# Kernel tuning notes

Measured on AMD Instinct MI355X. Metric: run time of the kernel, lower is better.

Reference implementation:

```python
import jax, jax.numpy as jnp
import numpy as np

EPS = 1e-5

def _ln(x, g=None, b=None):
    m = jnp.mean(x, axis=-1, keepdims=True)
    v = jnp.var(x, axis=-1, keepdims=True)
    y = (x - m) / jnp.sqrt(v + EPS)
    if g is not None:
        y = y * g + b
    return y

def setup_inputs() -> dict:
    key = jax.random.key(0)
    B, N, C = 2, 2048, 1024   # batch, tokens, query_dim
    H, D = 16, 64             # heads, dim_head -> inner = 1024
    inner = H * D
    ks = jax.random.split(key, 8)
    s = C ** -0.5
    inp = {
        'x':   jax.random.normal(ks[0], (B, N, C), jnp.float32),
        'w_q': jax.random.normal(ks[1], (C, inner), jnp.float32) * s,
        'b_q': jnp.zeros((inner,), jnp.float32),
        'w_k': jax.random.normal(ks[2], (C, inner), jnp.float32) * s,
        'b_k': jnp.zeros((inner,), jnp.float32),
        'w_v': jax.random.normal(ks[3], (C, inner), jnp.float32) * s,
        'b_v': jnp.zeros((inner,), jnp.float32),
        'g_q': jnp.ones((inner,), jnp.float32),
        'be_q': jnp.zeros((inner,), jnp.float32),
        'g_k': jnp.ones((inner,), jnp.float32),
        'be_k': jnp.zeros((inner,), jnp.float32),
        # to_out is zero-initialized in the torch code; use small random weights
        # so forward/backward are non-trivial for correctness testing.
        'w_o': jax.random.normal(ks[4], (inner, C), jnp.float32) * s,
        'b_o': jnp.zeros((C,), jnp.float32),
    }
    return inp

def reference(x, w_q, b_q, w_k, b_k, w_v, b_v, g_q, be_q, g_k, be_k, w_o, b_o):
    B, N, C = x.shape
    inner = w_q.shape[1]
    H = 16
    D = inner // H
    xn = _ln(x)                                  # pre-norm, no affine
    ctx = xn                                     # self-attention (context=None)
    silu = jax.nn.silu
    q = silu(xn) @ w_q + b_q                     # [B,N,inner]
    k = silu(ctx) @ w_k + b_k
    v = silu(ctx) @ w_v + b_v
    q = _ln(q, g_q, be_q)
    k = _ln(k, g_k, be_k)
    q = q * (inner ** -0.5)                      # NB: scale by inner_dim, pre-split
    q = q.reshape(B, N, H, D)
    k = k.reshape(B, N, H, D)
    v = v.reshape(B, N, H, D)
    w = jnp.einsum('bihd,bjhd->bhij', q, k)      # [B,H,N,N]
    w = jax.nn.softmax(w, axis=-1)
    o = jnp.einsum('bhij,bjhd->bihd', w, v).reshape(B, N, inner)
    return silu(o) @ w_o + b_o
```

## Files before the change

### kernel.cpp

```cpp
#include <hip/hip_runtime.h>
#include <hip/hip_bf16.h>
#include <math.h>

#define LN_EPS 1e-5f

typedef __attribute__((ext_vector_type(8))) short bf16x8;
typedef __attribute__((ext_vector_type(8))) short short8;
typedef __attribute__((ext_vector_type(4))) float f32x4;
typedef unsigned short ushort_t;

__device__ __forceinline__ float silu_f(float x) {
    return x / (1.0f + __expf(-x));
}

__device__ __forceinline__ ushort_t f2bf(float f) {
    __hip_bfloat16 h = __float2bfloat16(f);
    return *reinterpret_cast<ushort_t*>(&h);
}

__device__ __forceinline__ float bf2f(ushort_t u) {
    __hip_bfloat16 h = *reinterpret_cast<__hip_bfloat16*>(&u);
    return __bfloat162float(h);
}

__device__ __forceinline__ unsigned pk2(float a, float b) {
#if defined(__has_builtin)
#if __has_builtin(__builtin_amdgcn_cvt_pk_bf16_f32)
    return __builtin_bit_cast(unsigned, __builtin_amdgcn_cvt_pk_bf16_f32(a, b));
#else
    return (((unsigned)f2bf(b)) << 16) | (unsigned)f2bf(a);
#endif
#else
    return (((unsigned)f2bf(b)) << 16) | (unsigned)f2bf(a);
#endif
}

__device__ __forceinline__ void gld16(const void* g, void* lds) {
    __builtin_amdgcn_global_load_lds(
        (const __attribute__((address_space(1))) unsigned int*)g,
        (__attribute__((address_space(3))) unsigned int*)lds, 16, 0, 0);
}

__device__ __forceinline__ float2 block_reduce2(float2 p, float2* sbuf) {
    #pragma unroll
    for (int off = 32; off > 0; off >>= 1) {
        p.x += __shfl_down(p.x, off, 64);
        p.y += __shfl_down(p.y, off, 64);
    }
    int lane = threadIdx.x & 63;
    int wid  = threadIdx.x >> 6;
    if (lane == 0) sbuf[wid] = p;
    __syncthreads();
    if (threadIdx.x == 0) {
        float2 r = sbuf[0];
        for (int i = 1; i < 4; ++i) { r.x += sbuf[i].x; r.y += sbuf[i].y; }
        sbuf[0] = r;
    }
    __syncthreads();
    return sbuf[0];
}

__global__ __launch_bounds__(256) void ln_silu_kernel(
    const float* __restrict__ x, ushort_t* __restrict__ out)
{
    __shared__ float2 sbuf[4];
    const int C = 1024;
    int row = blockIdx.x;
    const float4* xr = (const float4*)(x + (size_t)row * C);
    float4 v = xr[threadIdx.x];
    float2 p;
    p.x = v.x + v.y + v.z + v.w;
    p.y = v.x*v.x + v.y*v.y + v.z*v.z + v.w*v.w;
    float2 s = block_reduce2(p, sbuf);
    float mean = s.x / (float)C;
    float var  = s.y / (float)C - mean * mean;
    float rstd = rsqrtf(var + LN_EPS);
    ushort4 y;
    y.x = f2bf(silu_f((v.x - mean) * rstd));
    y.y = f2bf(silu_f((v.y - mean) * rstd));
    y.z = f2bf(silu_f((v.z - mean) * rstd));
    y.w = f2bf(silu_f((v.w - mean) * rstd));
    ((ushort4*)(out + (size_t)row * C))[threadIdx.x] = y;
}

__global__ __launch_bounds__(256) void ln_affine_bf16(
    ushort_t* __restrict__ qk0, ushort_t* __restrict__ qk1,
    const float* __restrict__ g0, const float* __restrict__ be0,
    const float* __restrict__ g1, const float* __restrict__ be1,
    float scale0, float scale1)
{
    __shared__ float2 sbuf[4];
    const int C = 1024;
    int which = blockIdx.y;
    ushort_t* q = which ? qk1 : qk0;
    const float* g  = which ? g1  : g0;
    const float* be = which ? be1 : be0;
    float scale = which ? scale1 : scale0;
    int row = blockIdx.x;
    ushort4 u = ((ushort4*)(q + (size_t)row * C))[threadIdx.x];
    float v0 = bf2f(u.x), v1 = bf2f(u.y), v2 = bf2f(u.z), v3 = bf2f(u.w);
    float2 p;
    p.x = v0 + v1 + v2 + v3;
    p.y = v0*v0 + v1*v1 + v2*v2 + v3*v3;
    float2 s = block_reduce2(p, sbuf);
    float mean = s.x / (float)C;
    float var  = s.y / (float)C - mean * mean;
    float rstd = rsqrtf(var + LN_EPS);
    float4 gv = ((const float4*)g)[threadIdx.x];
    float4 bv = ((const float4*)be)[threadIdx.x];
    ushort4 y;
    y.x = f2bf(((v0 - mean) * rstd * gv.x + bv.x) * scale);
    y.y = f2bf(((v1 - mean) * rstd * gv.y + bv.y) * scale);
    y.z = f2bf(((v2 - mean) * rstd * gv.z + bv.z) * scale);
    y.w = f2bf(((v3 - mean) * rstd * gv.w + bv.w) * scale);
    ((ushort4*)(q + (size_t)row * C))[threadIdx.x] = y;
}

struct W4 { const float* p[4]; };

__global__ __launch_bounds__(256) void transpose_w(W4 w, ushort_t* __restrict__ outbase)
{
    __shared__ float Ls[64][65];
    int z = blockIdx.z;
    const float* in = w.p[z];
    ushort_t* out = outbase + (size_t)z * 1024 * 1024;
    int r0 = blockIdx.y * 64, c0 = blockIdx.x * 64;
    int t = threadIdx.x, r = t >> 2, j = (t & 3) * 16;
    #pragma unroll
    for (int i = 0; i < 4; ++i) {
        float4 v = *(const float4*)(in + (size_t)(r0 + r) * 1024 + c0 + j + i * 4);
        Ls[r][j + i*4 + 0] = v.x;
        Ls[r][j + i*4 + 1] = v.y;
        Ls[r][j + i*4 + 2] = v.z;
        Ls[r][j + i*4 + 3] = v.w;
    }
    __syncthreads();
    __align__(16) ushort_t tmp[16];
    #pragma unroll
    for (int i = 0; i < 16; ++i) tmp[i] = f2bf(Ls[j + i][r]);
    ushort_t* op = out + (size_t)(c0 + r) * 1024 + r0 + j;
    *(short8*)(op)     = *(short8*)(tmp);
    *(short8*)(op + 8) = *(short8*)(tmp + 8);
}

template<int BM, bool OUT_BF16>
__global__ __launch_bounds__(256) void gemm_mfma(
    const ushort_t* __restrict__ A, const ushort_t* __restrict__ Bt0,
    const float* __restrict__ b0, const float* __restrict__ b1,
    const float* __restrict__ b2, void* __restrict__ out0,
    ushort_t* __restrict__ vt_out,
    int M, int N, int K)
{
    constexpr int BK = 64;
    constexpr int MI = BM / 32;
    __shared__ ushort_t Smem[(BM + 128) * BK];
    ushort_t* As = Smem;
    ushort_t* Bs = Smem + BM * BK;

    int z = blockIdx.z;
    const ushort_t* Bt = Bt0 + (size_t)z * N * K;
    const float* bias = (z == 0) ? b0 : (z == 1) ? b1 : b2;

    int t = threadIdx.x;
    int lane = t & 63, wv = t >> 6;
    int wr = wv >> 1, wc = wv & 1;
    int quad = lane >> 4, ln16 = lane & 15;

    int row0 = blockIdx.y * BM;
    int col0 = blockIdx.x * 128;

    const f32x4 zero4 = {0.f, 0.f, 0.f, 0.f};
    f32x4 acc[MI][4];
    #pragma unroll
    for (int i = 0; i < MI; ++i)
        #pragma unroll
        for (int j = 0; j < 4; ++j) acc[i][j] = zero4;

    for (int kt = 0; kt < K; kt += BK) {
        #pragma unroll
        for (int c = 0; c < BM / 32; ++c) {
            int idx = c * 256 + t;
            int r = idx >> 3, ch = idx & 7;
            int g = ch ^ (r & 7);
            gld16(A + (size_t)(row0 + r) * K + kt + g * 8,
                  As + (size_t)(c * 256 + wv * 64) * 8);
        }
        #pragma unroll
        for (int c = 0; c < 4; ++c) {
            int idx = c * 256 + t;
            int r = idx >> 3, ch = idx & 7;
            int g = ch ^ (r & 7);
            gld16(Bt + (size_t)(col0 + r) * K + kt + g * 8,
                  Bs + (size_t)(c * 256 + wv * 64) * 8);
        }
        __syncthreads();
        #pragma unroll
        for (int s = 0; s < 2; ++s) {
            bf16x8 af[MI], bf[4];
            int g = s * 4 + quad;
            #pragma unroll
            for (int i = 0; i < MI; ++i) {
                int m = wr * (BM / 2) + i * 16 + ln16;
                af[i] = *(const bf16x8*)(As + (size_t)(m * 8 + (g ^ (m & 7))) * 8);
            }
            #pragma unroll
            for (int j = 0; j < 4; ++j) {
                int n = wc * 64 + j * 16 + ln16;
                bf[j] = *(const bf16x8*)(Bs + (size_t)(n * 8 + (g ^ (n & 7))) * 8);
            }
            #pragma unroll
            for (int i = 0; i < MI; ++i)
                #pragma unroll
                for (int j = 0; j < 4; ++j)
                    acc[i][j] = __builtin_amdgcn_mfma_f32_16x16x32_bf16(
                        af[i], bf[j], acc[i][j], 0, 0, 0);
        }
        __syncthreads();
    }

    if (OUT_BF16 && z == 2 && BM == 128) {
        ushort_t* tb = Smem + wv * 4096;
        int tok0 = row0 + wr * 64;
        int chn0 = col0 + wc * 64;
        #pragma unroll
        for (int j = 0; j < 4; ++j) {
            int chl = j * 16 + ln16;
            float bv = bias[chn0 + chl];
            #pragma unroll
            for (int i = 0; i < MI; ++i) {
                uint2 uu;
                uu.x = pk2(acc[i][j][0] + bv, acc[i][j][1] + bv);
                uu.y = pk2(acc[i][j][2] + bv, acc[i][j][3] + bv);
                int hc = i * 4 + quad;
                int phys = hc ^ ((chl & 7) << 1);
                *(uint2*)(tb + chl * 64 + phys * 4) = uu;
            }
        }
        int bb2 = tok0 >> 11;
        int tokb = tok0 & 2047;
        #pragma unroll
        for (int p = 0; p < 8; ++p) {
            int chl = p * 8 + (lane >> 3);
            int tc  = lane & 7;
            int ptc = tc ^ (chl & 7);
            uint4 vvv = *(const uint4*)(tb + chl * 64 + ptc * 8);
            *(uint4*)(vt_out + ((size_t)bb2 * 1024 + chn0 + chl) * 2048 + tokb + tc * 8) = vvv;
        }
    } else {
        #pragma unroll
        for (int j = 0; j < 4; ++j) {
            int col = col0 + wc * 64 + j * 16 + ln16;
            float bv = bias[col];
            #pragma unroll
            for (int i = 0; i < MI; ++i) {
                int rowb = row0 + wr * (BM / 2) + i * 16 + quad * 4;
                #pragma unroll
                for (int r = 0; r < 4; ++r) {
                    float val = acc[i][j][r] + bv;
                    if (OUT_BF16) {
                        ushort_t* out = (ushort_t*)out0 + (size_t)z * M * N;
                        out[(size_t)(rowb + r) * N + col] = f2bf(val);
                    } else {
                        float* out = (float*)out0;
                        out[(size_t)(rowb + r) * N + col] = val;
                    }
                }
            }
        }
    }
}

__global__ __launch_bounds__(256, 4) void flash_mfma(
    const ushort_t* __restrict__ qb, const ushort_t* __restrict__ kb,
    const ushort_t* __restrict__ vT, ushort_t* __restrict__ ob)
{
    const int N = 2048, HD = 1024, D = 64, H = 16;
    const int KT = 64;
    const int NT = N / KT;
    __shared__ ushort_t Ks[2][64 * 64];
    __shared__ ushort_t Vs[2][64 * 64];

    int t = threadIdx.x, lane = t & 63, wv = t >> 6;
    int quad = lane >> 4, ln16 = lane & 15;
    int qt = blockIdx.x, h = blockIdx.y, b = blockIdx.z;

    size_t qk_base = (size_t)b * N * HD + (size_t)h * D;
    size_t vt_base = (size_t)(b * H + h) * D * N;

    bf16x8 qf[2];
    {
        const ushort_t* qp = qb + qk_base + (size_t)(qt * 64 + wv * 16 + ln16) * HD;
        qf[0] = *(const bf16x8*)(qp + quad * 8);
        qf[1] = *(const bf16x8*)(qp + 32 + quad * 8);
    }

    const f32x4 zero4 = {0.f, 0.f, 0.f, 0.f};
    f32x4 oacc[4];
    #pragma unroll
    for (int j = 0; j < 4; ++j) oacc[j] = zero4;
    float lcur = 0.f;

    auto stage_tile = [&](ushort_t* KsB, ushort_t* VsB, int kt) {
        #pragma unroll
        for (int c = 0; c < 2; ++c) {
            int idx = c * 256 + t;
            int r = idx >> 3, ch = idx & 7, g = ch ^ (r & 7);
            int pr = (r & ~31) | (((r >> 2) & 3) << 3) | (((r >> 4) & 1) << 2) | (r & 3);
            gld16(kb + qk_base + (size_t)(kt + pr) * HD + g * 8,
                  KsB + (size_t)(c * 256 + wv * 64) * 8);
        }
        #pragma unroll
        for (int c = 0; c < 2; ++c) {
            int idx = c * 256 + t;
            int r = idx >> 3, ch = idx & 7, g = ch ^ (r & 7);
            gld16(vT + vt_base + (size_t)r * N + kt + g * 8,
                  VsB + (size_t)(c * 256 + wv * 64) * 8);
        }
    };

    auto compute_tile = [&](const ushort_t* KsB, const ushort_t* VsB) {
        f32x4 st[4];
        #pragma unroll
        for (int j = 0; j < 4; ++j) st[j] = zero4;
        __builtin_amdgcn_s_setprio(1);
        #pragma unroll
        for (int s = 0; s < 2; ++s) {
            int g = s * 4 + quad;
            #pragma unroll
            for (int j = 0; j < 4; ++j) {
                int n = j * 16 + ln16;
                bf16x8 kf = *(const bf16x8*)(KsB + ((size_t)n * 8 + (g ^ (n & 7))) * 8);
                st[j] = __builtin_amdgcn_mfma_f32_16x16x32_bf16(kf, qf[s], st[j], 0, 0, 0);
            }
        }
        __builtin_amdgcn_s_setprio(0);

        #pragma unroll
        for (int j = 0; j < 4; ++j) {
            st[j][0] = exp2f(st[j][0]);
            st[j][1] = exp2f(st[j][1]);
            st[j][2] = exp2f(st[j][2]);
            st[j][3] = exp2f(st[j][3]);
            lcur += (st[j][0] + st[j][1]) + (st[j][2] + st[j][3]);
        }

        #pragma unroll
        for (int w = 0; w < 2; ++w) {
            uint4 up;
            up.x = pk2(st[2*w][0],   st[2*w][1]);
            up.y = pk2(st[2*w][2],   st[2*w][3]);
            up.z = pk2(st[2*w+1][0], st[2*w+1][1]);
            up.w = pk2(st[2*w+1][2], st[2*w+1][3]);
            bf16x8 pf = __builtin_bit_cast(bf16x8, up);
            int lc = w * 4 + quad;
            int phys = lc ^ (ln16 & 7);
            __builtin_amdgcn_s_setprio(1);
            #pragma unroll
            for (int mt = 0; mt < 4; ++mt) {
                int dd = mt * 16 + ln16;
                bf16x8 vf = *(const bf16x8*)(VsB + (size_t)dd * 64 + phys * 8);
                oacc[mt] = __builtin_amdgcn_mfma_f32_16x16x32_bf16(vf, pf, oacc[mt], 0, 0, 0);
            }
            __builtin_amdgcn_s_setprio(0);
        }
        __builtin_amdgcn_sched_barrier(0);
    };

    stage_tile(Ks[0], Vs[0], 0);
    #pragma unroll 1
    for (int it = 0; it < NT; it += 2) {
        stage_tile(Ks[1], Vs[1], (it + 1) * KT);
        asm volatile("s_waitcnt vmcnt(4)" ::: "memory");
        __builtin_amdgcn_s_barrier();
        __builtin_amdgcn_sched_barrier(0);
        compute_tile(Ks[0], Vs[0]);
        __builtin_amdgcn_s_barrier();

        if (it + 2 < NT) {
            stage_tile(Ks[0], Vs[0], (it + 2) * KT);
            asm volatile("s_waitcnt vmcnt(4)" ::: "memory");
        } else {
            asm volatile("s_waitcnt vmcnt(0)" ::: "memory");
        }
        __builtin_amdgcn_s_barrier();
        __builtin_amdgcn_sched_barrier(0);
        compute_tile(Ks[1], Vs[1]);
        __builtin_amdgcn_s_barrier();
    }

    lcur += __shfl_xor(lcur, 16, 64);
    lcur += __shfl_xor(lcur, 32, 64);

    float inv = 1.0f / lcur;
    size_t rowoff = qk_base + (size_t)(qt * 64 + wv * 16 + ln16) * HD;
    #pragma unroll
    for (int mt = 0; mt < 4; ++mt) {
        float o0 = silu_f(oacc[mt][0] * inv);
        float o1 = silu_f(oacc[mt][1] * inv);
        float o2 = silu_f(oacc[mt][2] * inv);
        float o3 = silu_f(oacc[mt][3] * inv);
        uint2 uu;
        uu.x = pk2(o0, o1);
        uu.y = pk2(o2, o3);
        *(uint2*)(ob + rowoff + mt * 16 + quad * 4) = uu;
    }
}

extern "C" void kernel_launch(void* const* d_in, const int* in_sizes, int n_in,
                              void* d_out, int out_size, void* d_ws, size_t ws_size,
                              hipStream_t stream) {
    const float* x    = (const float*)d_in[0];
    const float* w_q  = (const float*)d_in[1];
    const float* b_q  = (const float*)d_in[2];
    const float* w_k  = (const float*)d_in[3];
    const float* b_k  = (const float*)d_in[4];
    const float* w_v  = (const float*)d_in[5];
    const float* b_v  = (const float*)d_in[6];
    const float* g_q  = (const float*)d_in[7];
    const float* be_q = (const float*)d_in[8];
    const float* g_k  = (const float*)d_in[9];
    const float* be_k = (const float*)d_in[10];
    const float* w_o  = (const float*)d_in[11];
    const float* b_o  = (const float*)d_in[12];
    float* out = (float*)d_out;

    const int B = 2, N = 2048, C = 1024, H = 16, INNER = 1024;
    const int M = B * N;
    const size_t MC = (size_t)M * C;

    ushort_t* ws  = (ushort_t*)d_ws;
    ushort_t* sx  = ws;
    ushort_t* qkv = ws + MC;
    ushort_t* vTp = ws + 4 * MC;
    ushort_t* wT  = ws + 5 * MC;

    ushort_t* qbuf = qkv;
    ushort_t* kbuf = qkv + MC;
    ushort_t* obuf = sx;

    W4 w4; w4.p[0] = w_q; w4.p[1] = w_k; w4.p[2] = w_v; w4.p[3] = w_o;
    transpose_w<<<dim3(16, 16, 4), 256, 0, stream>>>(w4, wT);

    ln_silu_kernel<<<M, 256, 0, stream>>>(x, sx);

    gemm_mfma<128, true><<<dim3(INNER / 128, M / 128, 3), 256, 0, stream>>>(
        sx, wT, b_q, b_k, b_v, qkv, vTp, M, INNER, C);

    ln_affine_bf16<<<dim3(M, 2), 256, 0, stream>>>(
        qbuf, kbuf, g_q, be_q, g_k, be_k, 0.03125f * 1.44269504f, 1.0f);

    flash_mfma<<<dim3(N / 64, H, B), 256, 0, stream>>>(qbuf, kbuf, vTp, obuf);

    gemm_mfma<64, false><<<dim3(C / 128, M / 64, 1), 256, 0, stream>>>(
        obuf, wT + (size_t)3 * 1024 * 1024, b_o, b_o, b_o, out, nullptr, M, C, INNER);
}
```

Baseline: 240.8 us.

## Process two query sub-tiles per wave and compute row sums via MFMA

Each wave now handles 32 query rows instead of 16, so every K and V fragment read from LDS is reused for two MFMAs, and each block covers 128 queries. This halves the grid and the K/V staging traffic per query. The softmax denominator is now accumulated with an MFMA against a ones vector on the bf16-rounded probabilities, replacing the VALU adds and cross-lane shuffles. Register pressure roughly doubles, so launch bounds drop to 2 blocks per SM. The grid also falls to 512 blocks, which may reduce occupancy and latency hiding.

```diff
diff --git a/kernel.cpp b/kernel.cpp
--- a/kernel.cpp
+++ b/kernel.cpp
@@ -270,7 +270,7 @@
     }
 }
 
-__global__ __launch_bounds__(256, 4) void flash_mfma(
+__global__ __launch_bounds__(256, 2) void flash_mfma(
     const ushort_t* __restrict__ qb, const ushort_t* __restrict__ kb,
     const ushort_t* __restrict__ vT, ushort_t* __restrict__ ob)
 {
@@ -287,18 +287,28 @@
     size_t qk_base = (size_t)b * N * HD + (size_t)h * D;
     size_t vt_base = (size_t)(b * H + h) * D * N;
 
-    bf16x8 qf[2];
-    {
-        const ushort_t* qp = qb + qk_base + (size_t)(qt * 64 + wv * 16 + ln16) * HD;
-        qf[0] = *(const bf16x8*)(qp + quad * 8);
-        qf[1] = *(const bf16x8*)(qp + 32 + quad * 8);
-    }
+    bf16x8 qf[2][2];
+    #pragma unroll
+    for (int u = 0; u < 2; ++u) {
+        const ushort_t* qp = qb + qk_base +
+            (size_t)(qt * 128 + wv * 32 + u * 16 + ln16) * HD;
+        qf[u][0] = *(const bf16x8*)(qp + quad * 8);
+        qf[u][1] = *(const bf16x8*)(qp + 32 + quad * 8);
+    }
+
+    bf16x8 ones;
+    #pragma unroll
+    for (int i = 0; i < 8; ++i) ones[i] = (short)0x3F80;
 
     const f32x4 zero4 = {0.f, 0.f, 0.f, 0.f};
-    f32x4 oacc[4];
-    #pragma unroll
-    for (int j = 0; j < 4; ++j) oacc[j] = zero4;
-    float lcur = 0.f;
+    f32x4 oacc[2][4];
+    f32x4 lacc[2];
+    #pragma unroll
+    for (int u = 0; u < 2; ++u) {
+        lacc[u] = zero4;
+        #pragma unroll
+        for (int j = 0; j < 4; ++j) oacc[u][j] = zero4;
+    }
 
     auto stage_tile = [&](ushort_t* KsB, ushort_t* VsB, int kt) {
         #pragma unroll
@@ -319,9 +329,11 @@
     };
 
     auto compute_tile = [&](const ushort_t* KsB, const ushort_t* VsB) {
-        f32x4 st[4];
-        #pragma unroll
-        for (int j = 0; j < 4; ++j) st[j] = zero4;
+        f32x4 st[2][4];
+        #pragma unroll
+        for (int u = 0; u < 2; ++u)
+            #pragma unroll
+            for (int j = 0; j < 4; ++j) st[u][j] = zero4;
         __builtin_amdgcn_s_setprio(1);
         #pragma unroll
         for (int s = 0; s < 2; ++s) {
@@ -330,36 +342,45 @@
             for (int j = 0; j < 4; ++j) {
                 int n = j * 16 + ln16;
                 bf16x8 kf = *(const bf16x8*)(KsB + ((size_t)n * 8 + (g ^ (n & 7))) * 8);
-                st[j] = __builtin_amdgcn_mfma_f32_16x16x32_bf16(kf, qf[s], st[j], 0, 0, 0);
+                st[0][j] = __builtin_amdgcn_mfma_f32_16x16x32_bf16(kf, qf[0][s], st[0][j], 0, 0, 0);
+                st[1][j] = __builtin_amdgcn_mfma_f32_16x16x32_bf16(kf, qf[1][s], st[1][j], 0, 0, 0);
             }
         }
         __builtin_amdgcn_s_setprio(0);
 
         #pragma unroll
-        for (int j = 0; j < 4; ++j) {
-            st[j][0] = exp2f(st[j][0]);
-            st[j][1] = exp2f(st[j][1]);
-            st[j][2] = exp2f(st[j][2]);
-            st[j][3] = exp2f(st[j][3]);
-            lcur += (st[j][0] + st[j][1]) + (st[j][2] + st[j][3]);
-        }
+        for (int u = 0; u < 2; ++u)
+            #pragma unroll
+            for (int j = 0; j < 4; ++j) {
+                st[u][j][0] = exp2f(st[u][j][0]);
+                st[u][j][1] = exp2f(st[u][j][1]);
+                st[u][j][2] = exp2f(st[u][j][2]);
+                st[u][j][3] = exp2f(st[u][j][3]);
+            }
 
         #pragma unroll
         for (int w = 0; w < 2; ++w) {
-            uint4 up;
-            up.x = pk2(st[2*w][0],   st[2*w][1]);
-            up.y = pk2(st[2*w][2],   st[2*w][3]);
-            up.z = pk2(st[2*w+1][0], st[2*w+1][1]);
-            up.w = pk2(st[2*w+1][2], st[2*w+1][3]);
-            bf16x8 pf = __builtin_bit_cast(bf16x8, up);
+            bf16x8 pf[2];
+            #pragma unroll
+            for (int u = 0; u < 2; ++u) {
+                uint4 up;
+                up.x = pk2(st[u][2*w][0],   st[u][2*w][1]);
+                up.y = pk2(st[u][2*w][2],   st[u][2*w][3]);
+                up.z = pk2(st[u][2*w+1][0], st[u][2*w+1][1]);
+                up.w = pk2(st[u][2*w+1][2], st[u][2*w+1][3]);
+                pf[u] = __builtin_bit_cast(bf16x8, up);
+            }
             int lc = w * 4 + quad;
             int phys = lc ^ (ln16 & 7);
             __builtin_amdgcn_s_setprio(1);
+            lacc[0] = __builtin_amdgcn_mfma_f32_16x16x32_bf16(ones, pf[0], lacc[0], 0, 0, 0);
+            lacc[1] = __builtin_amdgcn_mfma_f32_16x16x32_bf16(ones, pf[1], lacc[1], 0, 0, 0);
             #pragma unroll
             for (int mt = 0; mt < 4; ++mt) {
                 int dd = mt * 16 + ln16;
                 bf16x8 vf = *(const bf16x8*)(VsB + (size_t)dd * 64 + phys * 8);
-                oacc[mt] = __builtin_amdgcn_mfma_f32_16x16x32_bf16(vf, pf, oacc[mt], 0, 0, 0);
+                oacc[0][mt] = __builtin_amdgcn_mfma_f32_16x16x32_bf16(vf, pf[0], oacc[0][mt], 0, 0, 0);
+                oacc[1][mt] = __builtin_amdgcn_mfma_f32_16x16x32_bf16(vf, pf[1], oacc[1][mt], 0, 0, 0);
             }
             __builtin_amdgcn_s_setprio(0);
         }
@@ -388,21 +409,22 @@
         __builtin_amdgcn_s_barrier();
     }
 
-    lcur += __shfl_xor(lcur, 16, 64);
-    lcur += __shfl_xor(lcur, 32, 64);
-
-    float inv = 1.0f / lcur;
-    size_t rowoff = qk_base + (size_t)(qt * 64 + wv * 16 + ln16) * HD;
-    #pragma unroll
-    for (int mt = 0; mt < 4; ++mt) {
-        float o0 = silu_f(oacc[mt][0] * inv);
-        float o1 = silu_f(oacc[mt][1] * inv);
-        float o2 = silu_f(oacc[mt][2] * inv);
-        float o3 = silu_f(oacc[mt][3] * inv);
-        uint2 uu;
-        uu.x = pk2(o0, o1);
-        uu.y = pk2(o2, o3);
-        *(uint2*)(ob + rowoff + mt * 16 + quad * 4) = uu;
+    #pragma unroll
+    for (int u = 0; u < 2; ++u) {
+        float inv = 1.0f / lacc[u][0];
+        size_t rowoff = qk_base +
+            (size_t)(qt * 128 + wv * 32 + u * 16 + ln16) * HD;
+        #pragma unroll
+        for (int mt = 0; mt < 4; ++mt) {
+            float o0 = silu_f(oacc[u][mt][0] * inv);
+            float o1 = silu_f(oacc[u][mt][1] * inv);
+            float o2 = silu_f(oacc[u][mt][2] * inv);
+            float o3 = silu_f(oacc[u][mt][3] * inv);
+            uint2 uu;
+            uu.x = pk2(o0, o1);
+            uu.y = pk2(o2, o3);
+            *(uint2*)(ob + rowoff + mt * 16 + quad * 4) = uu;
+        }
     }
 }
 
@@ -449,7 +471,7 @@
     ln_affine_bf16<<<dim3(M, 2), 256, 0, stream>>>(
         qbuf, kbuf, g_q, be_q, g_k, be_k, 0.03125f * 1.44269504f, 1.0f);
 
-    flash_mfma<<<dim3(N / 64, H, B), 256, 0, stream>>>(qbuf, kbuf, vTp, obuf);
+    flash_mfma<<<dim3(N / 128, H, B), 256, 0, stream>>>(qbuf, kbuf, vTp, obuf);
 
     gemm_mfma<64, false><<<dim3(C / 128, M / 64, 1), 256, 0, stream>>>(
         obuf, wT + (size_t)3 * 1024 * 1024, b_o, b_o, b_o, out, nullptr, M, C, INNER);
```

Measured after the change: 240.1 us. No clear change (-0.3%).

## Software-pipeline attention QK and PV across tiles, MFMA row-sum, fast exp2

Applied to the files above, without the earlier changes.

Restructures the attention loop so each tile's QK^T MFMAs are overlapped with the previous tile's softmax and PV MFMAs. K and V staging are split so each can be refilled as soon as its buffer is free. The softmax denominator is now accumulated with an extra MFMA against a ones vector, which removes the scalar adds and the cross-lane shuffles. The change also switches to the hardware exp2 builtin and inline-asm bf16 packing, and hoists the V fragment loads. In exchange it holds two score register sets and has more complex waitcnt and barrier sequencing. The row sum is also now taken from bf16-rounded probabilities.

```diff
diff --git a/kernel.cpp b/kernel.cpp
--- a/kernel.cpp
+++ b/kernel.cpp
@@ -24,14 +24,20 @@
 }
 
 __device__ __forceinline__ unsigned pk2(float a, float b) {
+    unsigned r;
+    asm("v_cvt_pk_bf16_f32 %0, %1, %2" : "=v"(r) : "v"(a), "v"(b));
+    return r;
+}
+
+__device__ __forceinline__ float fast_exp2(float x) {
 #if defined(__has_builtin)
-#if __has_builtin(__builtin_amdgcn_cvt_pk_bf16_f32)
-    return __builtin_bit_cast(unsigned, __builtin_amdgcn_cvt_pk_bf16_f32(a, b));
+#if __has_builtin(__builtin_amdgcn_exp2f)
+    return __builtin_amdgcn_exp2f(x);
 #else
-    return (((unsigned)f2bf(b)) << 16) | (unsigned)f2bf(a);
+    return exp2f(x);
 #endif
 #else
-    return (((unsigned)f2bf(b)) << 16) | (unsigned)f2bf(a);
+    return exp2f(x);
 #endif
 }
 
@@ -294,13 +300,17 @@
         qf[1] = *(const bf16x8*)(qp + 32 + quad * 8);
     }
 
+    bf16x8 ones;
+    #pragma unroll
+    for (int i = 0; i < 8; ++i) ones[i] = (short)0x3F80;
+
     const f32x4 zero4 = {0.f, 0.f, 0.f, 0.f};
     f32x4 oacc[4];
+    f32x4 lacc = zero4;
     #pragma unroll
     for (int j = 0; j < 4; ++j) oacc[j] = zero4;
-    float lcur = 0.f;
-
-    auto stage_tile = [&](ushort_t* KsB, ushort_t* VsB, int kt) {
+
+    auto stage_K = [&](ushort_t* KsB, int kt) {
         #pragma unroll
         for (int c = 0; c < 2; ++c) {
             int idx = c * 256 + t;
@@ -309,6 +319,8 @@
             gld16(kb + qk_base + (size_t)(kt + pr) * HD + g * 8,
                   KsB + (size_t)(c * 256 + wv * 64) * 8);
         }
+    };
+    auto stage_V = [&](ushort_t* VsB, int kt) {
         #pragma unroll
         for (int c = 0; c < 2; ++c) {
             int idx = c * 256 + t;
@@ -318,8 +330,7 @@
         }
     };
 
-    auto compute_tile = [&](const ushort_t* KsB, const ushort_t* VsB) {
-        f32x4 st[4];
+    auto qk_tile = [&](const ushort_t* KsB, f32x4 (&st)[4]) {
         #pragma unroll
         for (int j = 0; j < 4; ++j) st[j] = zero4;
         __builtin_amdgcn_s_setprio(1);
@@ -334,16 +345,24 @@
             }
         }
         __builtin_amdgcn_s_setprio(0);
-
+    };
+
+    auto sm_pv = [&](f32x4 (&st)[4], const ushort_t* VsB) {
+        bf16x8 vf[2][4];
+        #pragma unroll
+        for (int w = 0; w < 2; ++w) {
+            int phys = (w * 4 + quad) ^ (ln16 & 7);
+            #pragma unroll
+            for (int mt = 0; mt < 4; ++mt)
+                vf[w][mt] = *(const bf16x8*)(VsB + (size_t)(mt * 16 + ln16) * 64 + phys * 8);
+        }
         #pragma unroll
         for (int j = 0; j < 4; ++j) {
-            st[j][0] = exp2f(st[j][0]);
-            st[j][1] = exp2f(st[j][1]);
-            st[j][2] = exp2f(st[j][2]);
-            st[j][3] = exp2f(st[j][3]);
-            lcur += (st[j][0] + st[j][1]) + (st[j][2] + st[j][3]);
-        }
-
+            st[j][0] = fast_exp2(st[j][0]);
+            st[j][1] = fast_exp2(st[j][1]);
+            st[j][2] = fast_exp2(st[j][2]);
+            st[j][3] = fast_exp2(st[j][3]);
+        }
         #pragma unroll
         for (int w = 0; w < 2; ++w) {
             uint4 up;
@@ -352,46 +371,60 @@
             up.z = pk2(st[2*w+1][0], st[2*w+1][1]);
             up.w = pk2(st[2*w+1][2], st[2*w+1][3]);
             bf16x8 pf = __builtin_bit_cast(bf16x8, up);
-            int lc = w * 4 + quad;
-            int phys = lc ^ (ln16 & 7);
             __builtin_amdgcn_s_setprio(1);
-            #pragma unroll
-            for (int mt = 0; mt < 4; ++mt) {
-                int dd = mt * 16 + ln16;
-                bf16x8 vf = *(const bf16x8*)(VsB + (size_t)dd * 64 + phys * 8);
-                oacc[mt] = __builtin_amdgcn_mfma_f32_16x16x32_bf16(vf, pf, oacc[mt], 0, 0, 0);
-            }
+            lacc = __builtin_amdgcn_mfma_f32_16x16x32_bf16(ones, pf, lacc, 0, 0, 0);
+            #pragma unroll
+            for (int mt = 0; mt < 4; ++mt)
+                oacc[mt] = __builtin_amdgcn_mfma_f32_16x16x32_bf16(vf[w][mt], pf, oacc[mt], 0, 0, 0);
             __builtin_amdgcn_s_setprio(0);
         }
-        __builtin_amdgcn_sched_barrier(0);
     };
 
-    stage_tile(Ks[0], Vs[0], 0);
+    f32x4 stA[4], stB[4];
+
+    stage_K(Ks[0], 0);       stage_V(Vs[0], 0);
+    stage_K(Ks[1], KT);      stage_V(Vs[1], KT);
+    asm volatile("s_waitcnt vmcnt(4)" ::: "memory");
+    __builtin_amdgcn_s_barrier();
+    __builtin_amdgcn_sched_barrier(0);
+    qk_tile(Ks[0], stA);
+    __builtin_amdgcn_sched_barrier(0);
+    __builtin_amdgcn_s_barrier();
+
     #pragma unroll 1
-    for (int it = 0; it < NT; it += 2) {
-        stage_tile(Ks[1], Vs[1], (it + 1) * KT);
+    for (int it = 0; it < NT - 2; it += 2) {
+        stage_K(Ks[0], (it + 2) * KT);
         asm volatile("s_waitcnt vmcnt(4)" ::: "memory");
         __builtin_amdgcn_s_barrier();
         __builtin_amdgcn_sched_barrier(0);
-        compute_tile(Ks[0], Vs[0]);
+        qk_tile(Ks[1], stB);
+        sm_pv(stA, Vs[0]);
+        __builtin_amdgcn_sched_barrier(0);
         __builtin_amdgcn_s_barrier();
-
-        if (it + 2 < NT) {
-            stage_tile(Ks[0], Vs[0], (it + 2) * KT);
-            asm volatile("s_waitcnt vmcnt(4)" ::: "memory");
-        } else {
-            asm volatile("s_waitcnt vmcnt(0)" ::: "memory");
-        }
+        stage_V(Vs[0], (it + 2) * KT);
+
+        stage_K(Ks[1], (it + 3) * KT);
+        asm volatile("s_waitcnt vmcnt(4)" ::: "memory");
         __builtin_amdgcn_s_barrier();
         __builtin_amdgcn_sched_barrier(0);
-        compute_tile(Ks[1], Vs[1]);
+        qk_tile(Ks[0], stA);
+        sm_pv(stB, Vs[1]);
+        __builtin_amdgcn_sched_barrier(0);
         __builtin_amdgcn_s_barrier();
-    }
-
-    lcur += __shfl_xor(lcur, 16, 64);
-    lcur += __shfl_xor(lcur, 32, 64);
-
-    float inv = 1.0f / lcur;
+        stage_V(Vs[1], (it + 3) * KT);
+    }
+
+    asm volatile("s_waitcnt vmcnt(2)" ::: "memory");
+    __builtin_amdgcn_s_barrier();
+    __builtin_amdgcn_sched_barrier(0);
+    qk_tile(Ks[1], stB);
+    sm_pv(stA, Vs[0]);
+    asm volatile("s_waitcnt vmcnt(0)" ::: "memory");
+    __builtin_amdgcn_s_barrier();
+    __builtin_amdgcn_sched_barrier(0);
+    sm_pv(stB, Vs[1]);
+
+    float inv = 1.0f / lacc[0];
     size_t rowoff = qk_base + (size_t)(qt * 64 + wv * 16 + ln16) * HD;
     #pragma unroll
     for (int mt = 0; mt < 4; ++mt) {
```

Result: faster. 227.7 us (-5.4%).
